# Optimization experiments

Measured on AMD Instinct MI355X. Metric: run time of the kernel, lower is better.

## Reference

```python
import jax, jax.numpy as jnp
import numpy as np
import jax.scipy.linalg as jsl

EPS = 1e-3
GROUP_SIZE = 16

def setup_inputs() -> dict:
    key = jax.random.key(0)
    x = jax.random.normal(key, (32, 512, 56, 56), dtype=jnp.float32)
    return {"x": x}

def reference(x):
    B, C, H, W = x.shape
    gs = GROUP_SIZE
    G = C // gs
    # batch mean per channel: mean over (B, H, W)
    m = jnp.mean(x, axis=(0, 2, 3), keepdims=True)  # [1, C, 1, 1]
    xn = x - m
    # [C, B, H, W] -> [G, gs, N] with N = B*H*W
    T = jnp.transpose(xn, (1, 0, 2, 3)).reshape(G, gs, -1)
    N = T.shape[-1]
    f_cov = jnp.einsum('gin,gjn->gij', T, T) / N  # [G, gs, gs]
    eye = jnp.eye(gs, dtype=x.dtype)
    f_cov_shrinked = (1.0 - EPS) * f_cov + EPS * eye
    L = jnp.linalg.cholesky(f_cov_shrinked)  # lower triangular, L L^T = cov
    # inverse of L via triangular solve against identity (batched)
    Linv = jsl.solve_triangular(L, jnp.broadcast_to(eye, (G, gs, gs)), lower=True)
    # grouped 1x1 conv == per-group matmul: out_g = Linv_g @ xn_g
    dec = jnp.einsum('gij,gjn->gin', Linv, T)  # [G, gs, N]
    out = jnp.transpose(dec.reshape(C, B, H, W), (1, 0, 2, 3))
    return out
```

## Files before the change

### kernel.cpp

```cpp
#include <hip/hip_runtime.h>
#include <hip/hip_bf16.h>
#include <math.h>

#define Bb 32
#define Cc 512
#define HW 3136
#define HW4 784
#define G  32
#define GS 16
#define Nn (Bb*HW)
#define EPSF 1e-3f
#define TRI 136
#define STATS (TRI+GS)

typedef float floatx4 __attribute__((ext_vector_type(4)));

#define TIDX(i,j) ((i)*GS - (i)*((i)+1)/2 + (j))

__global__ __launch_bounds__(256) void stats_kernel(const float* __restrict__ x,
                                                    float* __restrict__ part) {
    const int blk = blockIdx.x;
    const int b = blk / G;
    const int g = blk % G;
    const floatx4* __restrict__ xb4 = reinterpret_cast<const floatx4*>(
        x + ((size_t)b * Cc + (size_t)g * GS) * HW);

    float s[GS];
    float c[TRI];
#pragma unroll
    for (int i = 0; i < GS; i++) s[i] = 0.f;
#pragma unroll
    for (int i = 0; i < TRI; i++) c[i] = 0.f;

    for (int p = threadIdx.x; p < HW4; p += 256) {
        floatx4 v[GS];
#pragma unroll
        for (int j = 0; j < GS; j++) v[j] = xb4[(size_t)j * HW4 + p];
#pragma unroll
        for (int j = 0; j < GS; j++) s[j] += (v[j].x + v[j].y) + (v[j].z + v[j].w);
#pragma unroll
        for (int i = 0; i < GS; i++) {
#pragma unroll
            for (int j = i; j < GS; j++) {
                float acc = c[TIDX(i, j)];
                acc = fmaf(v[i].x, v[j].x, acc);
                acc = fmaf(v[i].y, v[j].y, acc);
                acc = fmaf(v[i].z, v[j].z, acc);
                acc = fmaf(v[i].w, v[j].w, acc);
                c[TIDX(i, j)] = acc;
            }
        }
    }

#pragma unroll
    for (int m = 1; m < 64; m <<= 1) {
#pragma unroll
        for (int i = 0; i < GS; i++) s[i] += __shfl_xor(s[i], m, 64);
#pragma unroll
        for (int i = 0; i < TRI; i++) c[i] += __shfl_xor(c[i], m, 64);
    }

    __shared__ float red[4][STATS];
    const int wave = threadIdx.x >> 6;
    const int lane = threadIdx.x & 63;
    if (lane == 0) {
#pragma unroll
        for (int i = 0; i < GS; i++) red[wave][i] = s[i];
#pragma unroll
        for (int i = 0; i < TRI; i++) red[wave][GS + i] = c[i];
    }
    __syncthreads();
    if (threadIdx.x < STATS) {
        float t = red[0][threadIdx.x] + red[1][threadIdx.x] +
                  red[2][threadIdx.x] + red[3][threadIdx.x];
        part[((size_t)g * Bb + b) * STATS + threadIdx.x] = t;
    }
}

__global__ __launch_bounds__(64) void solve_kernel(const float* __restrict__ part,
                                                   float* __restrict__ wl) {
    const int g = blockIdx.x;
    const int t = threadIdx.x;

    __shared__ float st[STATS];
    __shared__ float Lsh[GS][GS + 1];
    __shared__ float Ish[GS][GS + 1];

    for (int k = t; k < STATS; k += 64) {
        float acc = 0.f;
#pragma unroll
        for (int b = 0; b < Bb; b++)
            acc += part[((size_t)g * Bb + b) * STATS + k];
        st[k] = acc;
    }
    __syncthreads();

    const float invN = 1.0f / (float)Nn;

    if (t < GS) {
        float A[GS];
        const float mi = st[t] * invN;
#pragma unroll
        for (int j = 0; j < GS; j++) {
            const int ii = t < j ? t : j;
            const int jj = t < j ? j : t;
            const float mj = st[j] * invN;
            float cv = st[GS + TIDX(ii, jj)] * invN - mi * mj;
            cv *= (1.0f - EPSF);
            if (j == t) cv += EPSF;
            A[j] = cv;
        }

#pragma unroll
        for (int k = 0; k < GS; k++) {
            const float dkk = __shfl(A[k], k, 64);
            const float d = sqrtf(dkk);
            const float lik = (t == k) ? d : A[k] / d;
            A[k] = lik;
#pragma unroll
            for (int j = k + 1; j < GS; j++) {
                const float ljk = __shfl(A[k], j, 64);
                A[j] -= lik * ljk;
            }
        }

#pragma unroll
        for (int j = 0; j < GS; j++) Lsh[t][j] = A[j];
    }
    __syncthreads();

    if (t < GS) {
        const int j = t;
        float col[GS];
#pragma unroll
        for (int i = 0; i < GS; i++) col[i] = 0.f;
#pragma unroll
        for (int i = 0; i < GS; i++) {
            float v = (i == j) ? 1.f : 0.f;
#pragma unroll
            for (int k = 0; k < i; k++) v -= Lsh[i][k] * col[k];
            col[i] = (i >= j) ? v / Lsh[i][i] : 0.f;
        }
#pragma unroll
        for (int i = 0; i < GS; i++) Ish[i][j] = col[i];
    }
    __syncthreads();

    float* wg = wl + (size_t)g * STATS;
    for (int e = t; e < GS * GS; e += 64) {
        const int i = e >> 4, j = e & 15;
        if (j <= i) wg[i * (i + 1) / 2 + j] = Ish[i][j];
    }
    if (t < GS) {
        float bias = 0.f;
#pragma unroll
        for (int j = 0; j < GS; j++) bias += Ish[t][j] * (st[j] * invN);
        wg[TRI + t] = bias;
    }
}

__global__ __launch_bounds__(256) void apply_kernel(const float* __restrict__ x,
                                                    const float* __restrict__ wl,
                                                    float* __restrict__ out) {
    const int blk = blockIdx.x;
    const int b = blk / G;
    const int g = blk % G;

    const float* __restrict__ wg = wl + (size_t)g * STATS;
    float Lt[TRI];
    float bias[GS];
#pragma unroll
    for (int i = 0; i < TRI; i++) Lt[i] = wg[i];
#pragma unroll
    for (int i = 0; i < GS; i++) bias[i] = wg[TRI + i];

    const size_t base_off = ((size_t)b * Cc + (size_t)g * GS) * HW;
    const floatx4* __restrict__ xb4 = reinterpret_cast<const floatx4*>(x + base_off);
    floatx4* __restrict__ ob4 = reinterpret_cast<floatx4*>(out + base_off);

    for (int p = threadIdx.x; p < HW4; p += 256) {
        floatx4 v[GS];
#pragma unroll
        for (int j = 0; j < GS; j++) v[j] = xb4[(size_t)j * HW4 + p];
#pragma unroll
        for (int i = 0; i < GS; i++) {
            floatx4 o = (floatx4)(-bias[i]);
#pragma unroll
            for (int j = 0; j <= i; j++) {
                o += Lt[i * (i + 1) / 2 + j] * v[j];
            }
            __builtin_nontemporal_store(o, &ob4[(size_t)i * HW4 + p]);
        }
    }
}

extern "C" void kernel_launch(void* const* d_in, const int* in_sizes, int n_in,
                              void* d_out, int out_size, void* d_ws, size_t ws_size,
                              hipStream_t stream) {
    const float* x = (const float*)d_in[0];
    float* out = (float*)d_out;

    float* part = (float*)d_ws;
    float* wl = part + (size_t)G * Bb * STATS;

    stats_kernel<<<Bb * G, 256, 0, stream>>>(x, part);
    solve_kernel<<<G, 64, 0, stream>>>(part, wl);
    apply_kernel<<<Bb * G, 256, 0, stream>>>(x, wl, out);
}
```

Measured before the change: 425.4 us.

## Compute group covariance with bf16 split-precision MFMA in stats kernel

Rewrites the statistics kernel so each wave loads 16 channel rows and builds the 16x16 Gram matrix with MFMA 16x16x32 bf16 instructions. Each value is split into a hi and a lo bf16 part, and the hi*hi and hi*lo products are accumulated to approximate fp32 accuracy. The cross terms are then symmetrised through LDS across 8 waves of a 512-thread block. This replaces the large register-heavy scalar FMA triangle (136 accumulators plus shuffles) that limited occupancy, at the cost of slightly lower covariance precision since the lo*lo term is dropped.

```diff
diff --git a/kernel.cpp b/kernel.cpp
--- a/kernel.cpp
+++ b/kernel.cpp
@@ -12,68 +12,90 @@
 #define EPSF 1e-3f
 #define TRI 136
 #define STATS (TRI+GS)
+#define NCHUNK 98
 
 typedef float floatx4 __attribute__((ext_vector_type(4)));
+typedef short bf16x8 __attribute__((ext_vector_type(8)));
 
 #define TIDX(i,j) ((i)*GS - (i)*((i)+1)/2 + (j))
 
-__global__ __launch_bounds__(256) void stats_kernel(const float* __restrict__ x,
-                                                    float* __restrict__ part) {
+__device__ __forceinline__ unsigned short f32_bf16_rne(float f) {
+    unsigned u = __builtin_bit_cast(unsigned, f);
+    unsigned r = u + 0x7fffu + ((u >> 16) & 1u);
+    return (unsigned short)(r >> 16);
+}
+__device__ __forceinline__ float bf16_f32(unsigned short h) {
+    unsigned u = ((unsigned)h) << 16;
+    return __builtin_bit_cast(float, u);
+}
+
+__global__ __launch_bounds__(512, 8) void stats_kernel(const float* __restrict__ x,
+                                                       float* __restrict__ part) {
     const int blk = blockIdx.x;
     const int b = blk / G;
     const int g = blk % G;
-    const floatx4* __restrict__ xb4 = reinterpret_cast<const floatx4*>(
-        x + ((size_t)b * Cc + (size_t)g * GS) * HW);
-
-    float s[GS];
-    float c[TRI];
-#pragma unroll
-    for (int i = 0; i < GS; i++) s[i] = 0.f;
-#pragma unroll
-    for (int i = 0; i < TRI; i++) c[i] = 0.f;
-
-    for (int p = threadIdx.x; p < HW4; p += 256) {
-        floatx4 v[GS];
-#pragma unroll
-        for (int j = 0; j < GS; j++) v[j] = xb4[(size_t)j * HW4 + p];
-#pragma unroll
-        for (int j = 0; j < GS; j++) s[j] += (v[j].x + v[j].y) + (v[j].z + v[j].w);
-#pragma unroll
-        for (int i = 0; i < GS; i++) {
-#pragma unroll
-            for (int j = i; j < GS; j++) {
-                float acc = c[TIDX(i, j)];
-                acc = fmaf(v[i].x, v[j].x, acc);
-                acc = fmaf(v[i].y, v[j].y, acc);
-                acc = fmaf(v[i].z, v[j].z, acc);
-                acc = fmaf(v[i].w, v[j].w, acc);
-                c[TIDX(i, j)] = acc;
-            }
-        }
-    }
-
-#pragma unroll
-    for (int m = 1; m < 64; m <<= 1) {
-#pragma unroll
-        for (int i = 0; i < GS; i++) s[i] += __shfl_xor(s[i], m, 64);
-#pragma unroll
-        for (int i = 0; i < TRI; i++) c[i] += __shfl_xor(c[i], m, 64);
-    }
-
-    __shared__ float red[4][STATS];
-    const int wave = threadIdx.x >> 6;
-    const int lane = threadIdx.x & 63;
-    if (lane == 0) {
-#pragma unroll
-        for (int i = 0; i < GS; i++) red[wave][i] = s[i];
-#pragma unroll
-        for (int i = 0; i < TRI; i++) red[wave][GS + i] = c[i];
-    }
-    __syncthreads();
-    if (threadIdx.x < STATS) {
-        float t = red[0][threadIdx.x] + red[1][threadIdx.x] +
-                  red[2][threadIdx.x] + red[3][threadIdx.x];
-        part[((size_t)g * Bb + b) * STATS + threadIdx.x] = t;
+    const int tid = threadIdx.x;
+    const int w = tid >> 6;
+    const int lane = tid & 63;
+    const int row = lane & 15;
+    const int kgrp = lane >> 4;
+
+    const float* __restrict__ base =
+        x + ((size_t)b * Cc + (size_t)g * GS + row) * HW + kgrp * 8;
+
+    floatx4 acc_hh = {0.f, 0.f, 0.f, 0.f};
+    floatx4 acc_hl = {0.f, 0.f, 0.f, 0.f};
+    float s_acc = 0.f;
+
+    for (int t = w; t < NCHUNK; t += 8) {
+        const float* p = base + t * 32;
+        const floatx4 v0 = *reinterpret_cast<const floatx4*>(p);
+        const floatx4 v1 = *reinterpret_cast<const floatx4*>(p + 4);
+
+        bf16x8 hi, lo;
+#pragma unroll
+        for (int e = 0; e < 8; e++) {
+            const float f = (e < 4) ? v0[e] : v1[e - 4];
+            const unsigned short hb = f32_bf16_rne(f);
+            const float lf = f - bf16_f32(hb);
+            hi[e] = (short)hb;
+            lo[e] = (short)f32_bf16_rne(lf);
+            s_acc += f;
+        }
+        acc_hh = __builtin_amdgcn_mfma_f32_16x16x32_bf16(hi, hi, acc_hh, 0, 0, 0);
+        acc_hl = __builtin_amdgcn_mfma_f32_16x16x32_bf16(hi, lo, acc_hl, 0, 0, 0);
+    }
+
+    s_acc += __shfl_xor(s_acc, 16, 64);
+    s_acc += __shfl_xor(s_acc, 32, 64);
+
+    __shared__ float lds_hh[8][GS][GS];
+    __shared__ float lds_hl[8][GS][GS];
+    __shared__ float lds_s[8][GS];
+#pragma unroll
+    for (int r = 0; r < 4; r++) {
+        lds_hh[w][kgrp * 4 + r][row] = acc_hh[r];
+        lds_hl[w][kgrp * 4 + r][row] = acc_hl[r];
+    }
+    if (lane < GS) lds_s[w][lane] = s_acc;
+    __syncthreads();
+
+    float* __restrict__ pb = part + ((size_t)g * Bb + b) * STATS;
+    if (tid < 256) {
+        const int i = tid >> 4, j = tid & 15;
+        if (j >= i) {
+            float v = 0.f;
+#pragma unroll
+            for (int ww = 0; ww < 8; ww++)
+                v += lds_hh[ww][i][j] + lds_hl[ww][i][j] + lds_hl[ww][j][i];
+            pb[GS + TIDX(i, j)] = v;
+        }
+        if (tid < GS) {
+            float sv = 0.f;
+#pragma unroll
+            for (int ww = 0; ww < 8; ww++) sv += lds_s[ww][tid];
+            pb[tid] = sv;
+        }
     }
 }
 
@@ -203,7 +225,7 @@
     float* part = (float*)d_ws;
     float* wl = part + (size_t)G * Bb * STATS;
 
-    stats_kernel<<<Bb * G, 256, 0, stream>>>(x, part);
+    stats_kernel<<<Bb * G, 512, 0, stream>>>(x, part);
     solve_kernel<<<G, 64, 0, stream>>>(part, wl);
     apply_kernel<<<Bb * G, 256, 0, stream>>>(x, wl, out);
 }
```

Result: faster. 384.0 us (-9.7%).
